# Performance work log

Hardware: AMD Instinct MI355X
Metric: run time of the kernel (lower is better)

## Reference

```python
import jax, jax.numpy as jnp
import numpy as np
import math

B, T, D, H = 2, 2048, 1024, 16
DK = D // H


def _alibi_bias(n_heads, seq_len):
    # canonical ALiBi: slope_h = 2^(-8*(h+1)/n_heads), bias[h,i,j] = -slope_h * (i - j) for j<=i
    slopes = jnp.asarray([2.0 ** (-8.0 * (h + 1) / n_heads) for h in range(n_heads)], dtype=jnp.float32)
    pos = jnp.arange(seq_len, dtype=jnp.float32)
    dist = pos[None, :] - pos[:, None]              # [T, T], (j - i)
    return slopes[:, None, None] * dist[None, :, :]  # [H, T, T] (masked out above diagonal anyway)


def setup_inputs() -> dict:
    key = jax.random.key(0)
    ks = jax.random.split(key, 8)
    s = 1.0 / math.sqrt(D)
    return {
        "query": jax.random.normal(ks[0], (B, T, D), dtype=jnp.float32),
        "key": jax.random.normal(ks[1], (B, T, D), dtype=jnp.float32),
        "value": jax.random.normal(ks[2], (B, T, D), dtype=jnp.float32),
        "alibi_bias": _alibi_bias(H, T),
        "Wq": jax.random.normal(ks[3], (D, D), dtype=jnp.float32) * s,
        "Wk": jax.random.normal(ks[4], (D, D), dtype=jnp.float32) * s,
        "Wv": jax.random.normal(ks[5], (D, D), dtype=jnp.float32) * s,
        "Wo": jax.random.normal(ks[6], (D, D), dtype=jnp.float32) * s,
        "bo": jnp.zeros((D,), dtype=jnp.float32),
    }


def reference(query, key, value, alibi_bias, Wq, Wk, Wv, Wo, bo):
    b, tq, d = query.shape
    tk = key.shape[1]
    # projections (torch Linear: x @ W.T)
    Q = (query @ Wq.T).reshape(b, tq, H, DK).transpose(0, 2, 1, 3)  # [B,H,Tq,dk]
    K = (key @ Wk.T).reshape(b, tk, H, DK).transpose(0, 2, 1, 3)
    V = (value @ Wv.T).reshape(b, tk, H, DK).transpose(0, 2, 1, 3)
    scores = jnp.einsum("bhqd,bhkd->bhqk", Q, K) / math.sqrt(DK)   # [B,H,Tq,Tk]
    scores = scores + alibi_bias[None]
    causal = jnp.triu(jnp.ones((tq, tk), dtype=bool), 1)
    scores = jnp.where(causal, jnp.float32(-jnp.inf), scores)
    attn = jax.nn.softmax(scores, axis=-1)
    out = jnp.einsum("bhqk,bhkd->bhqd", attn, V)                   # [B,H,Tq,dk]
    out = out.transpose(0, 2, 1, 3).reshape(b, tq, d)
    return out @ Wo.T + bo
```

## Files before the change

kernel.cpp:

```cpp
#include <hip/hip_runtime.h>
#include <hip/hip_bf16.h>


#define B_  2
#define T_  2048
#define D_  1024
#define H_  16
#define DK_ 64
#define M_  (B_ * T_)

typedef unsigned short u16;
typedef __attribute__((ext_vector_type(8))) short bf16x8;
typedef __attribute__((ext_vector_type(4))) float f32x4;

__device__ __constant__ float d_slopes[16] = {
    0.70710678118654752440f, 0.5f, 0.35355339059327376220f, 0.25f,
    0.17677669529663688110f, 0.125f, 0.088388347648318440550f, 0.0625f,
    0.044194173824159220275f, 0.03125f, 0.022097086912079610137f, 0.015625f,
    0.011048543456039805068f, 0.0078125f, 0.0055242717280199025342f, 0.00390625f};

__device__ __forceinline__ u16 f2bf_bits(float v) {
    union { __hip_bfloat16 h; u16 u; } cv;
    cv.h = __float2bfloat16(v);
    return cv.u;
}

__device__ __forceinline__ void mfma_step(const u16* As, const u16* Bs,
                                          int wm, int wn, int l15, int quad,
                                          f32x4 acc[4][4]) {
    bf16x8 af[4], bf[4];
#pragma unroll
    for (int mi = 0; mi < 4; ++mi)
        af[mi] = *(const bf16x8*)&As[(wm * 64 + mi * 16 + l15) * 40 + quad * 8];
#pragma unroll
    for (int ni = 0; ni < 4; ++ni)
        bf[ni] = *(const bf16x8*)&Bs[(wn * 64 + ni * 16 + l15) * 40 + quad * 8];
#pragma unroll
    for (int mi = 0; mi < 4; ++mi)
#pragma unroll
        for (int ni = 0; ni < 4; ++ni)
            acc[mi][ni] = __builtin_amdgcn_mfma_f32_16x16x32_bf16(af[mi], bf[ni], acc[mi][ni], 0, 0, 0);
}

__global__ __launch_bounds__(256) void gemm_qkv(
    const float* __restrict__ xq, const float* __restrict__ xk, const float* __restrict__ xv,
    const float* __restrict__ wq, const float* __restrict__ wk, const float* __restrict__ wv,
    u16* __restrict__ oq, u16* __restrict__ ok, u16* __restrict__ ov) {
    __shared__ u16 smem[2 * 128 * 40];
    u16* As = smem;
    u16* Bs = smem + 128 * 40;

    const int z = blockIdx.z;
    const float* X = (z == 0) ? xq : (z == 1) ? xk : xv;
    const float* W = (z == 0) ? wq : (z == 1) ? wk : wv;

    const int tid = threadIdx.x;
    const int lane = tid & 63;
    const int l15 = lane & 15, quad = lane >> 4;
    const int wid = tid >> 6;
    const int wm = wid >> 1, wn = wid & 1;
    const int m0 = blockIdx.y * 128;
    const int n0 = blockIdx.x * 128;

    const int srow = tid >> 1;
    const int shalf = tid & 1;
    const float* xp0 = X + (size_t)(m0 + srow) * D_ + shalf * 16;
    const float* wp0 = W + (size_t)(n0 + srow) * D_ + shalf * 16;
    u16* asw = As + srow * 40 + shalf * 16;
    u16* bsw = Bs + srow * 40 + shalf * 16;

    f32x4 acc[4][4];
#pragma unroll
    for (int mi = 0; mi < 4; ++mi)
#pragma unroll
        for (int ni = 0; ni < 4; ++ni) acc[mi][ni] = f32x4{0.f, 0.f, 0.f, 0.f};

    for (int k0 = 0; k0 < D_; k0 += 32) {
        alignas(16) u16 ta[16], tb[16];
#pragma unroll
        for (int i = 0; i < 4; ++i) {
            float4 f = *(const float4*)(xp0 + k0 + i * 4);
            ta[i * 4 + 0] = f2bf_bits(f.x); ta[i * 4 + 1] = f2bf_bits(f.y);
            ta[i * 4 + 2] = f2bf_bits(f.z); ta[i * 4 + 3] = f2bf_bits(f.w);
        }
#pragma unroll
        for (int i = 0; i < 4; ++i) {
            float4 f = *(const float4*)(wp0 + k0 + i * 4);
            tb[i * 4 + 0] = f2bf_bits(f.x); tb[i * 4 + 1] = f2bf_bits(f.y);
            tb[i * 4 + 2] = f2bf_bits(f.z); tb[i * 4 + 3] = f2bf_bits(f.w);
        }
        __syncthreads();
        *(uint4*)asw = *(const uint4*)&ta[0];
        *(uint4*)(asw + 8) = *(const uint4*)&ta[8];
        *(uint4*)bsw = *(const uint4*)&tb[0];
        *(uint4*)(bsw + 8) = *(const uint4*)&tb[8];
        __syncthreads();
        mfma_step(As, Bs, wm, wn, l15, quad, acc);
    }

    if (z < 2) {
        u16* out = (z == 0) ? oq : ok;
#pragma unroll
        for (int mi = 0; mi < 4; ++mi) {
            const int gmb = m0 + wm * 64 + mi * 16 + quad * 4;
#pragma unroll
            for (int ni = 0; ni < 4; ++ni) {
                const int gn = n0 + wn * 64 + ni * 16 + l15;
                const int h = gn >> 6, dk = gn & 63;
#pragma unroll
                for (int r = 0; r < 4; ++r) {
                    const int gm = gmb + r;
                    const int b = gm >> 11, t = gm & (T_ - 1);
                    out[(((size_t)b * H_ + h) * T_ + t) * DK_ + dk] = f2bf_bits(acc[mi][ni][r]);
                }
            }
        }
    } else {
        u16* Cs = smem;
#pragma unroll
        for (int h2 = 0; h2 < 2; ++h2) {
            __syncthreads();
            if (wn == h2) {
#pragma unroll
                for (int mi = 0; mi < 4; ++mi) {
#pragma unroll
                    for (int ni = 0; ni < 4; ++ni) {
                        const int nloc = ni * 16 + l15;
                        const int mloc = wm * 64 + mi * 16 + quad * 4;
                        alignas(8) u16 pk[4];
#pragma unroll
                        for (int r = 0; r < 4; ++r) pk[r] = f2bf_bits(acc[mi][ni][r]);
                        *(uint2*)&Cs[nloc * 136 + mloc] = *(const uint2*)pk;
                    }
                }
            }
            __syncthreads();
            const int nr = tid >> 2;
            const int mseg = (tid & 3) * 32;
            const int gn = n0 + h2 * 64 + nr;
            const int h = gn >> 6, dk = gn & 63;
            const int b = m0 >> 11;
            const int tl = (m0 & (T_ - 1)) + mseg;
            uint4 v0 = *(const uint4*)&Cs[nr * 136 + mseg];
            uint4 v1 = *(const uint4*)&Cs[nr * 136 + mseg + 8];
            uint4 v2 = *(const uint4*)&Cs[nr * 136 + mseg + 16];
            uint4 v3 = *(const uint4*)&Cs[nr * 136 + mseg + 24];
            u16* op = ov + ((size_t)(b * H_ + h) * DK_ + dk) * T_ + tl;
            *(uint4*)op = v0; *(uint4*)(op + 8) = v1;
            *(uint4*)(op + 16) = v2; *(uint4*)(op + 24) = v3;
        }
    }
}

__global__ __launch_bounds__(256) void gemm_out(const u16* __restrict__ X,
                                                const float* __restrict__ W,
                                                const float* __restrict__ bias,
                                                float* __restrict__ out) {
    __shared__ u16 As[128 * 40];
    __shared__ u16 Bs[128 * 40];

    const int tid = threadIdx.x;
    const int lane = tid & 63;
    const int l15 = lane & 15, quad = lane >> 4;
    const int wid = tid >> 6;
    const int wm = wid >> 1, wn = wid & 1;
    const int m0 = blockIdx.y * 128;
    const int n0 = blockIdx.x * 128;

    const int srow = tid >> 1;
    const int shalf = tid & 1;
    const u16* xp0 = X + (size_t)(m0 + srow) * D_ + shalf * 16;
    const float* wp0 = W + (size_t)(n0 + srow) * D_ + shalf * 16;
    u16* asw = As + srow * 40 + shalf * 16;
    u16* bsw = Bs + srow * 40 + shalf * 16;

    f32x4 acc[4][4];
#pragma unroll
    for (int mi = 0; mi < 4; ++mi)
#pragma unroll
        for (int ni = 0; ni < 4; ++ni) acc[mi][ni] = f32x4{0.f, 0.f, 0.f, 0.f};

    for (int k0 = 0; k0 < D_; k0 += 32) {
        uint4 xa = *(const uint4*)(xp0 + k0);
        uint4 xb = *(const uint4*)(xp0 + k0 + 8);
        alignas(16) u16 tb[16];
#pragma unroll
        for (int i = 0; i < 4; ++i) {
            float4 f = *(const float4*)(wp0 + k0 + i * 4);
            tb[i * 4 + 0] = f2bf_bits(f.x); tb[i * 4 + 1] = f2bf_bits(f.y);
            tb[i * 4 + 2] = f2bf_bits(f.z); tb[i * 4 + 3] = f2bf_bits(f.w);
        }
        __syncthreads();
        *(uint4*)asw = xa;
        *(uint4*)(asw + 8) = xb;
        *(uint4*)bsw = *(const uint4*)&tb[0];
        *(uint4*)(bsw + 8) = *(const uint4*)&tb[8];
        __syncthreads();
        mfma_step(As, Bs, wm, wn, l15, quad, acc);
    }

#pragma unroll
    for (int mi = 0; mi < 4; ++mi) {
        const int gmb = m0 + wm * 64 + mi * 16 + quad * 4;
#pragma unroll
        for (int ni = 0; ni < 4; ++ni) {
            const int gn = n0 + wn * 64 + ni * 16 + l15;
            const float bv = bias[gn];
#pragma unroll
            for (int r = 0; r < 4; ++r)
                out[(size_t)(gmb + r) * D_ + gn] = acc[mi][ni][r] + bv;
        }
    }
}

__global__ __launch_bounds__(256) void flash_attn(const u16* __restrict__ Q,
                                                  const u16* __restrict__ K,
                                                  const u16* __restrict__ VT,
                                                  u16* __restrict__ ctx) {
    const int bh = blockIdx.x;
    const int b  = bh >> 4;
    const int h  = bh & 15;
    const int wave = threadIdx.x >> 6;
    const int lane = threadIdx.x & 63;
    const int l15 = lane & 15;
    const int quad = lane >> 4;
    const int qt = gridDim.y - 1 - blockIdx.y;
    const int qb = qt * 64 + wave * 16;
    const float slope = d_slopes[h];

    __shared__ u16 plds[4][16 * 168];
    u16* pl = plds[wave];

    const size_t baseQK = (size_t)bh * T_ * DK_;
    const u16* qptr = Q + baseQK + (size_t)(qb + l15) * DK_ + quad * 8;
    bf16x8 aq0 = *(const bf16x8*)qptr;
    bf16x8 aq1 = *(const bf16x8*)(qptr + 32);

    f32x4 o[4], osum;
#pragma unroll
    for (int t = 0; t < 4; ++t) o[t] = f32x4{0.f, 0.f, 0.f, 0.f};
    osum = f32x4{0.f, 0.f, 0.f, 0.f};

    const f32x4 zero = {0.f, 0.f, 0.f, 0.f};
    bf16x8 ones;
#pragma unroll
    for (int i = 0; i < 8; ++i) ones[i] = (short)0x3F80;

    for (int kb = 0; kb < qb + 16; kb += 128) {
        f32x4 s[8];
#pragma unroll
        for (int t = 0; t < 8; ++t) {
            const u16* kptr = K + baseQK + (size_t)(kb + t * 16 + l15) * DK_ + quad * 8;
            bf16x8 bk0 = *(const bf16x8*)kptr;
            bf16x8 bk1 = *(const bf16x8*)(kptr + 32);
            s[t] = __builtin_amdgcn_mfma_f32_16x16x32_bf16(aq0, bk0, zero, 0, 0, 0);
            s[t] = __builtin_amdgcn_mfma_f32_16x16x32_bf16(aq1, bk1, s[t], 0, 0, 0);
        }

#pragma unroll
        for (int t = 0; t < 8; ++t) {
#pragma unroll
            for (int r = 0; r < 4; ++r) {
                const int row = qb + quad * 4 + r;
                const int c = kb + t * 16 + l15;
                const float v = s[t][r] * 0.125f + slope * (float)(c - row);
                const float p = (c <= row) ? __expf(v) : 0.f;
                pl[(quad * 4 + r) * 168 + t * 16 + l15] = f2bf_bits(p);
            }
        }

        bf16x8 ap[4];
#pragma unroll
        for (int g = 0; g < 4; ++g)
            ap[g] = *(const bf16x8*)&pl[l15 * 168 + g * 32 + quad * 8];

#pragma unroll
        for (int t = 0; t < 4; ++t) {
            const u16* vbase = VT + ((size_t)bh * DK_ + t * 16 + l15) * T_ + kb;
#pragma unroll
            for (int g = 0; g < 4; ++g) {
                bf16x8 bv = *(const bf16x8*)(vbase + g * 32 + quad * 8);
                o[t] = __builtin_amdgcn_mfma_f32_16x16x32_bf16(ap[g], bv, o[t], 0, 0, 0);
            }
        }
#pragma unroll
        for (int g = 0; g < 4; ++g)
            osum = __builtin_amdgcn_mfma_f32_16x16x32_bf16(ap[g], ones, osum, 0, 0, 0);
    }

#pragma unroll
    for (int r = 0; r < 4; ++r) {
        const float inv = 1.0f / osum[r];
        const int row = qb + quad * 4 + r;
        u16* cp = ctx + ((size_t)b * T_ + row) * D_ + h * DK_ + l15;
#pragma unroll
        for (int t = 0; t < 4; ++t) cp[t * 16] = f2bf_bits(o[t][r] * inv);
    }
}

extern "C" void kernel_launch(void* const* d_in, const int* in_sizes, int n_in,
                              void* d_out, int out_size, void* d_ws, size_t ws_size,
                              hipStream_t stream) {
    const float* query = (const float*)d_in[0];
    const float* key   = (const float*)d_in[1];
    const float* value = (const float*)d_in[2];
    const float* Wq    = (const float*)d_in[4];
    const float* Wk    = (const float*)d_in[5];
    const float* Wv    = (const float*)d_in[6];
    const float* Wo    = (const float*)d_in[7];
    const float* bo    = (const float*)d_in[8];
    float* out = (float*)d_out;

    const size_t elems = (size_t)B_ * H_ * T_ * DK_;
    u16* Qb   = (u16*)d_ws;
    u16* Kb   = Qb + elems;
    u16* VTb  = Kb + elems;
    u16* ctxb = VTb + elems;

    dim3 blk(256);
    gemm_qkv<<<dim3(D_ / 128, M_ / 128, 3), blk, 0, stream>>>(query, key, value, Wq, Wk, Wv, Qb, Kb, VTb);
    flash_attn<<<dim3(B_ * H_, T_ / 64), blk, 0, stream>>>(Qb, Kb, VTb, ctxb);
    gemm_out<<<dim3(D_ / 128, M_ / 128), blk, 0, stream>>>(ctxb, Wo, bo, out);
}
```

Measured before the change: 616.2 us.

## Pre-convert inputs to bf16 and use direct global-to-LDS loads in GEMMs

```diff
diff --git a/kernel.cpp b/kernel.cpp
--- a/kernel.cpp
+++ b/kernel.cpp
@@ -13,6 +13,10 @@
 typedef __attribute__((ext_vector_type(8))) short bf16x8;
 typedef __attribute__((ext_vector_type(4))) float f32x4;
 
+#define GL16(g, l) __builtin_amdgcn_global_load_lds( \
+    (const __attribute__((address_space(1))) unsigned int*)(const void*)(g), \
+    (__attribute__((address_space(3))) unsigned int*)(void*)(l), 16, 0, 0)
+
 __device__ __constant__ float d_slopes[16] = {
     0.70710678118654752440f, 0.5f, 0.35355339059327376220f, 0.25f,
     0.17677669529663688110f, 0.125f, 0.088388347648318440550f, 0.0625f,
@@ -25,77 +29,79 @@
     return cv.u;
 }
 
-__device__ __forceinline__ void mfma_step(const u16* As, const u16* Bs,
-                                          int wm, int wn, int l15, int quad,
-                                          f32x4 acc[4][4]) {
-    bf16x8 af[4], bf[4];
+__global__ __launch_bounds__(256) void cvt_all(
+    const float* __restrict__ q, const float* __restrict__ k, const float* __restrict__ v,
+    const float* __restrict__ wq, const float* __restrict__ wk,
+    const float* __restrict__ wv, const float* __restrict__ wo,
+    u16* __restrict__ xq, u16* __restrict__ xk, u16* __restrict__ xv,
+    u16* __restrict__ uq, u16* __restrict__ uk, u16* __restrict__ uv, u16* __restrict__ uo) {
+    const int b = blockIdx.x;
+    const float* s; u16* d; int rel;
+    if      (b < 2048) { s = q;  d = xq; rel = b; }
+    else if (b < 4096) { s = k;  d = xk; rel = b - 2048; }
+    else if (b < 6144) { s = v;  d = xv; rel = b - 4096; }
+    else if (b < 6656) { s = wq; d = uq; rel = b - 6144; }
+    else if (b < 7168) { s = wk; d = uk; rel = b - 6656; }
+    else if (b < 7680) { s = wv; d = uv; rel = b - 7168; }
+    else               { s = wo; d = uo; rel = b - 7680; }
+    const size_t base = (size_t)rel * 2048 + threadIdx.x * 8;
+    float4 f0 = *(const float4*)(s + base);
+    float4 f1 = *(const float4*)(s + base + 4);
+    alignas(16) u16 o[8];
+    o[0] = f2bf_bits(f0.x); o[1] = f2bf_bits(f0.y); o[2] = f2bf_bits(f0.z); o[3] = f2bf_bits(f0.w);
+    o[4] = f2bf_bits(f1.x); o[5] = f2bf_bits(f1.y); o[6] = f2bf_bits(f1.z); o[7] = f2bf_bits(f1.w);
+    *(uint4*)(d + base) = *(const uint4*)o;
+}
+
+__global__ __launch_bounds__(256) void gemm_qkv(
+    const u16* __restrict__ xq, const u16* __restrict__ xk, const u16* __restrict__ xv,
+    const u16* __restrict__ wq, const u16* __restrict__ wk, const u16* __restrict__ wv,
+    u16* __restrict__ oq, u16* __restrict__ ok, u16* __restrict__ ov) {
+    __shared__ u16 smem[8704];
+    u16* As = smem;
+    u16* Bs = smem + 4096;
+
+    const int z = blockIdx.z;
+    const u16* X = (z == 0) ? xq : (z == 1) ? xk : xv;
+    const u16* W = (z == 0) ? wq : (z == 1) ? wk : wv;
+
+    const int tid = threadIdx.x, lane = tid & 63, w = tid >> 6;
+    const int l15 = lane & 15, quad = lane >> 4;
+    const int wm = w >> 1, wn = w & 1;
+    const int m0 = blockIdx.y * 128, n0 = blockIdx.x * 128;
+    const int srow = lane >> 2;
+    const int skseg = (lane & 3) * 8;
+
+    f32x4 acc[4][4];
 #pragma unroll
     for (int mi = 0; mi < 4; ++mi)
-        af[mi] = *(const bf16x8*)&As[(wm * 64 + mi * 16 + l15) * 40 + quad * 8];
-#pragma unroll
-    for (int ni = 0; ni < 4; ++ni)
-        bf[ni] = *(const bf16x8*)&Bs[(wn * 64 + ni * 16 + l15) * 40 + quad * 8];
-#pragma unroll
-    for (int mi = 0; mi < 4; ++mi)
+#pragma unroll
+        for (int ni = 0; ni < 4; ++ni) acc[mi][ni] = f32x4{0.f, 0.f, 0.f, 0.f};
+
+    const u16* ga = X + (size_t)(m0 + w * 32 + srow) * D_ + skseg;
+    const u16* gb = W + (size_t)(n0 + w * 32 + srow) * D_ + skseg;
+    u16* lA = As + (w * 32) * 32;
+    u16* lB = Bs + (w * 32) * 32;
+
+    for (int k0 = 0; k0 < D_; k0 += 32) {
+        GL16(ga + k0,             lA);
+        GL16(ga + k0 + 16 * D_,   lA + 16 * 32);
+        GL16(gb + k0,             lB);
+        GL16(gb + k0 + 16 * D_,   lB + 16 * 32);
+        __syncthreads();
+        bf16x8 af[4], bfr[4];
+#pragma unroll
+        for (int mi = 0; mi < 4; ++mi)
+            af[mi] = *(const bf16x8*)&As[(wm * 64 + mi * 16 + l15) * 32 + quad * 8];
 #pragma unroll
         for (int ni = 0; ni < 4; ++ni)
-            acc[mi][ni] = __builtin_amdgcn_mfma_f32_16x16x32_bf16(af[mi], bf[ni], acc[mi][ni], 0, 0, 0);
-}
-
-__global__ __launch_bounds__(256) void gemm_qkv(
-    const float* __restrict__ xq, const float* __restrict__ xk, const float* __restrict__ xv,
-    const float* __restrict__ wq, const float* __restrict__ wk, const float* __restrict__ wv,
-    u16* __restrict__ oq, u16* __restrict__ ok, u16* __restrict__ ov) {
-    __shared__ u16 smem[2 * 128 * 40];
-    u16* As = smem;
-    u16* Bs = smem + 128 * 40;
-
-    const int z = blockIdx.z;
-    const float* X = (z == 0) ? xq : (z == 1) ? xk : xv;
-    const float* W = (z == 0) ? wq : (z == 1) ? wk : wv;
-
-    const int tid = threadIdx.x;
-    const int lane = tid & 63;
-    const int l15 = lane & 15, quad = lane >> 4;
-    const int wid = tid >> 6;
-    const int wm = wid >> 1, wn = wid & 1;
-    const int m0 = blockIdx.y * 128;
-    const int n0 = blockIdx.x * 128;
-
-    const int srow = tid >> 1;
-    const int shalf = tid & 1;
-    const float* xp0 = X + (size_t)(m0 + srow) * D_ + shalf * 16;
-    const float* wp0 = W + (size_t)(n0 + srow) * D_ + shalf * 16;
-    u16* asw = As + srow * 40 + shalf * 16;
-    u16* bsw = Bs + srow * 40 + shalf * 16;
-
-    f32x4 acc[4][4];
-#pragma unroll
-    for (int mi = 0; mi < 4; ++mi)
-#pragma unroll
-        for (int ni = 0; ni < 4; ++ni) acc[mi][ni] = f32x4{0.f, 0.f, 0.f, 0.f};
-
-    for (int k0 = 0; k0 < D_; k0 += 32) {
-        alignas(16) u16 ta[16], tb[16];
-#pragma unroll
-        for (int i = 0; i < 4; ++i) {
-            float4 f = *(const float4*)(xp0 + k0 + i * 4);
-            ta[i * 4 + 0] = f2bf_bits(f.x); ta[i * 4 + 1] = f2bf_bits(f.y);
-            ta[i * 4 + 2] = f2bf_bits(f.z); ta[i * 4 + 3] = f2bf_bits(f.w);
-        }
-#pragma unroll
-        for (int i = 0; i < 4; ++i) {
-            float4 f = *(const float4*)(wp0 + k0 + i * 4);
-            tb[i * 4 + 0] = f2bf_bits(f.x); tb[i * 4 + 1] = f2bf_bits(f.y);
-            tb[i * 4 + 2] = f2bf_bits(f.z); tb[i * 4 + 3] = f2bf_bits(f.w);
-        }
+            bfr[ni] = *(const bf16x8*)&Bs[(wn * 64 + ni * 16 + l15) * 32 + quad * 8];
+#pragma unroll
+        for (int mi = 0; mi < 4; ++mi)
+#pragma unroll
+            for (int ni = 0; ni < 4; ++ni)
+                acc[mi][ni] = __builtin_amdgcn_mfma_f32_16x16x32_bf16(af[mi], bfr[ni], acc[mi][ni], 0, 0, 0);
         __syncthreads();
-        *(uint4*)asw = *(const uint4*)&ta[0];
-        *(uint4*)(asw + 8) = *(const uint4*)&ta[8];
-        *(uint4*)bsw = *(const uint4*)&tb[0];
-        *(uint4*)(bsw + 8) = *(const uint4*)&tb[8];
-        __syncthreads();
-        mfma_step(As, Bs, wm, wn, l15, quad, acc);
     }
 
     if (z < 2) {
@@ -153,58 +159,56 @@
 }
 
 __global__ __launch_bounds__(256) void gemm_out(const u16* __restrict__ X,
-                                                const float* __restrict__ W,
+                                                const u16* __restrict__ W,
                                                 const float* __restrict__ bias,
                                                 float* __restrict__ out) {
-    __shared__ u16 As[128 * 40];
-    __shared__ u16 Bs[128 * 40];
-
-    const int tid = threadIdx.x;
-    const int lane = tid & 63;
+    __shared__ u16 As[128 * 32];
+    __shared__ u16 Bs[64 * 32];
+
+    const int tid = threadIdx.x, lane = tid & 63, w = tid >> 6;
     const int l15 = lane & 15, quad = lane >> 4;
-    const int wid = tid >> 6;
-    const int wm = wid >> 1, wn = wid & 1;
-    const int m0 = blockIdx.y * 128;
-    const int n0 = blockIdx.x * 128;
-
-    const int srow = tid >> 1;
-    const int shalf = tid & 1;
-    const u16* xp0 = X + (size_t)(m0 + srow) * D_ + shalf * 16;
-    const float* wp0 = W + (size_t)(n0 + srow) * D_ + shalf * 16;
-    u16* asw = As + srow * 40 + shalf * 16;
-    u16* bsw = Bs + srow * 40 + shalf * 16;
-
-    f32x4 acc[4][4];
+    const int wm = w >> 1, wn = w & 1;
+    const int m0 = blockIdx.y * 128, n0 = blockIdx.x * 64;
+    const int srow = lane >> 2;
+    const int skseg = (lane & 3) * 8;
+
+    f32x4 acc[4][2];
 #pragma unroll
     for (int mi = 0; mi < 4; ++mi)
 #pragma unroll
-        for (int ni = 0; ni < 4; ++ni) acc[mi][ni] = f32x4{0.f, 0.f, 0.f, 0.f};
+        for (int ni = 0; ni < 2; ++ni) acc[mi][ni] = f32x4{0.f, 0.f, 0.f, 0.f};
+
+    const u16* ga = X + (size_t)(m0 + w * 32 + srow) * D_ + skseg;
+    const u16* gb = W + (size_t)(n0 + w * 16 + srow) * D_ + skseg;
+    u16* lA = As + (w * 32) * 32;
+    u16* lB = Bs + (w * 16) * 32;
 
     for (int k0 = 0; k0 < D_; k0 += 32) {
-        uint4 xa = *(const uint4*)(xp0 + k0);
-        uint4 xb = *(const uint4*)(xp0 + k0 + 8);
-        alignas(16) u16 tb[16];
-#pragma unroll
-        for (int i = 0; i < 4; ++i) {
-            float4 f = *(const float4*)(wp0 + k0 + i * 4);
-            tb[i * 4 + 0] = f2bf_bits(f.x); tb[i * 4 + 1] = f2bf_bits(f.y);
-            tb[i * 4 + 2] = f2bf_bits(f.z); tb[i * 4 + 3] = f2bf_bits(f.w);
-        }
+        GL16(ga + k0,           lA);
+        GL16(ga + k0 + 16 * D_, lA + 16 * 32);
+        GL16(gb + k0,           lB);
         __syncthreads();
-        *(uint4*)asw = xa;
-        *(uint4*)(asw + 8) = xb;
-        *(uint4*)bsw = *(const uint4*)&tb[0];
-        *(uint4*)(bsw + 8) = *(const uint4*)&tb[8];
+        bf16x8 af[4], bfr[2];
+#pragma unroll
+        for (int mi = 0; mi < 4; ++mi)
+            af[mi] = *(const bf16x8*)&As[(wm * 64 + mi * 16 + l15) * 32 + quad * 8];
+#pragma unroll
+        for (int ni = 0; ni < 2; ++ni)
+            bfr[ni] = *(const bf16x8*)&Bs[(wn * 32 + ni * 16 + l15) * 32 + quad * 8];
+#pragma unroll
+        for (int mi = 0; mi < 4; ++mi)
+#pragma unroll
+            for (int ni = 0; ni < 2; ++ni)
+                acc[mi][ni] = __builtin_amdgcn_mfma_f32_16x16x32_bf16(af[mi], bfr[ni], acc[mi][ni], 0, 0, 0);
         __syncthreads();
-        mfma_step(As, Bs, wm, wn, l15, quad, acc);
     }
 
 #pragma unroll
     for (int mi = 0; mi < 4; ++mi) {
         const int gmb = m0 + wm * 64 + mi * 16 + quad * 4;
 #pragma unroll
-        for (int ni = 0; ni < 4; ++ni) {
-            const int gn = n0 + wn * 64 + ni * 16 + l15;
+        for (int ni = 0; ni < 2; ++ni) {
+            const int gn = n0 + wn * 32 + ni * 16 + l15;
             const float bv = bias[gn];
 #pragma unroll
             for (int r = 0; r < 4; ++r)
@@ -213,10 +217,10 @@
     }
 }
 
-__global__ __launch_bounds__(256) void flash_attn(const u16* __restrict__ Q,
-                                                  const u16* __restrict__ K,
-                                                  const u16* __restrict__ VT,
-                                                  u16* __restrict__ ctx) {
+__global__ __launch_bounds__(256, 2) void flash_attn(const u16* __restrict__ Q,
+                                                     const u16* __restrict__ K,
+                                                     const u16* __restrict__ VT,
+                                                     u16* __restrict__ ctx) {
     const int bh = blockIdx.x;
     const int b  = bh >> 4;
     const int h  = bh & 15;
@@ -257,6 +261,15 @@
             s[t] = __builtin_amdgcn_mfma_f32_16x16x32_bf16(aq1, bk1, s[t], 0, 0, 0);
         }
 
+        bf16x8 vf[4][4];
+#pragma unroll
+        for (int t = 0; t < 4; ++t) {
+            const u16* vbase = VT + ((size_t)bh * DK_ + t * 16 + l15) * T_ + kb;
+#pragma unroll
+            for (int g = 0; g < 4; ++g)
+                vf[t][g] = *(const bf16x8*)(vbase + g * 32 + quad * 8);
+        }
+
 #pragma unroll
         for (int t = 0; t < 8; ++t) {
 #pragma unroll
@@ -275,14 +288,10 @@
             ap[g] = *(const bf16x8*)&pl[l15 * 168 + g * 32 + quad * 8];
 
 #pragma unroll
-        for (int t = 0; t < 4; ++t) {
-            const u16* vbase = VT + ((size_t)bh * DK_ + t * 16 + l15) * T_ + kb;
-#pragma unroll
-            for (int g = 0; g < 4; ++g) {
-                bf16x8 bv = *(const bf16x8*)(vbase + g * 32 + quad * 8);
-                o[t] = __builtin_amdgcn_mfma_f32_16x16x32_bf16(ap[g], bv, o[t], 0, 0, 0);
-            }
-        }
+        for (int t = 0; t < 4; ++t)
+#pragma unroll
+            for (int g = 0; g < 4; ++g)
+                o[t] = __builtin_amdgcn_mfma_f32_16x16x32_bf16(ap[g], vf[t][g], o[t], 0, 0, 0);
 #pragma unroll
         for (int g = 0; g < 4; ++g)
             osum = __builtin_amdgcn_mfma_f32_16x16x32_bf16(ap[g], ones, osum, 0, 0, 0);
@@ -311,14 +320,24 @@
     const float* bo    = (const float*)d_in[8];
     float* out = (float*)d_out;
 
-    const size_t elems = (size_t)B_ * H_ * T_ * DK_;
+    const size_t elems  = (size_t)B_ * H_ * T_ * DK_;
+    const size_t welems = (size_t)D_ * D_;
     u16* Qb   = (u16*)d_ws;
     u16* Kb   = Qb + elems;
     u16* VTb  = Kb + elems;
     u16* ctxb = VTb + elems;
+    u16* Xq   = ctxb + elems;
+    u16* Xk   = Xq + elems;
+    u16* Xv   = Xk + elems;
+    u16* Uq   = Xv + elems;
+    u16* Uk   = Uq + welems;
+    u16* Uv   = Uk + welems;
+    u16* Uo   = Uv + welems;
 
     dim3 blk(256);
-    gemm_qkv<<<dim3(D_ / 128, M_ / 128, 3), blk, 0, stream>>>(query, key, value, Wq, Wk, Wv, Qb, Kb, VTb);
+    cvt_all<<<8192, blk, 0, stream>>>(query, key, value, Wq, Wk, Wv, Wo,
+                                      Xq, Xk, Xv, Uq, Uk, Uv, Uo);
+    gemm_qkv<<<dim3(D_ / 128, M_ / 128, 3), blk, 0, stream>>>(Xq, Xk, Xv, Uq, Uk, Uv, Qb, Kb, VTb);
     flash_attn<<<dim3(B_ * H_, T_ / 64), blk, 0, stream>>>(Qb, Kb, VTb, ctxb);
-    gemm_out<<<dim3(D_ / 128, M_ / 128), blk, 0, stream>>>(ctxb, Wo, bo, out);
-}
+    gemm_out<<<dim3(D_ / 64, M_ / 128), blk, 0, stream>>>(ctxb, Uo, bo, out);
+}
```

Result: faster. 546.7 us (-11.3%).
